# Kernel tuning notes

Hardware: AMD Instinct MI355X
Metric: run time of the kernel (lower is better)

Reference implementation:

```python
import jax, jax.numpy as jnp
import numpy as np

N = 100000      # nodes
E = 1600000     # edges (avg degree 16)
IN = 128        # in_channels
H = 4           # heads
C = 32          # out_channels per head
NEG_SLOPE = 0.2 # PyG GATConv default


def setup_inputs() -> dict:
    key = jax.random.key(0)
    k = jax.random.split(key, 6)
    x = jax.random.normal(k[0], (N, IN), jnp.float32)
    edge_index = jax.random.randint(k[1], (2, E), 0, N, jnp.int32)
    # Learned params of GATConv: linear weight, per-head attention vectors, bias
    W = jax.random.normal(k[2], (IN, H * C), jnp.float32) / np.sqrt(IN)
    a_src = jax.random.normal(k[3], (H, C), jnp.float32) * 0.1
    a_dst = jax.random.normal(k[4], (H, C), jnp.float32) * 0.1
    bias = jnp.zeros((H * C,), jnp.float32)
    return {"x": x, "edge_index": edge_index, "W": W,
            "a_src": a_src, "a_dst": a_dst, "bias": bias}


def reference(x, edge_index, W, a_src, a_dst, bias):
    n = x.shape[0]
    # Linear transform, per-head view: [N, H, C]
    h = (x @ W).reshape(n, H, C)
    # Node-level attention halves: alpha_i = <h_i, a>  -> [N, H]
    alpha_src = jnp.einsum('nhc,hc->nh', h, a_src)
    alpha_dst = jnp.einsum('nhc,hc->nh', h, a_dst)
    # add_self_loops=True (PyG default)
    loops = jnp.arange(n, dtype=edge_index.dtype)
    src = jnp.concatenate([edge_index[0], loops])  # [E+N]
    dst = jnp.concatenate([edge_index[1], loops])
    # Edge attention logits with LeakyReLU: [E+N, H]
    e = jax.nn.leaky_relu(alpha_src[src] + alpha_dst[dst], NEG_SLOPE)
    # Numerically stable softmax over incoming edges of each destination node
    m = jax.ops.segment_max(e, dst, num_segments=n)          # [N, H]
    e = jnp.exp(e - m[dst])
    denom = jax.ops.segment_sum(e, dst, num_segments=n)      # [N, H]
    att = e / denom[dst]                                     # [E+N, H]
    # Weighted scatter-aggregate of source features: [N, H, C]
    out = jax.ops.segment_sum(att[:, :, None] * h[src], dst, num_segments=n)
    # concat=True: flatten heads, add bias
    return out.reshape(n, H * C) + bias
```

## Files before the change

kernel.cpp:

```cpp
#include <hip/hip_runtime.h>
#include <stdint.h>


#define NBLK 512
#define BKT 64
#define CAP 1792

typedef __bf16 bf16x8 __attribute__((ext_vector_type(8)));
typedef float f32x4 __attribute__((ext_vector_type(4)));

__device__ __forceinline__ float lrelu(float x) { return x >= 0.f ? x : 0.2f * x; }
__device__ __forceinline__ float blo(unsigned u) { return __uint_as_float(u << 16); }
__device__ __forceinline__ float bhi(unsigned u) { return __uint_as_float(u & 0xffff0000u); }
__device__ __forceinline__ unsigned pk2(float a, float b) {
  unsigned short ua = __builtin_bit_cast(unsigned short, (__bf16)a);
  unsigned short ub = __builtin_bit_cast(unsigned short, (__bf16)b);
  return ((unsigned)ub << 16) | ua;
}

__global__ __launch_bounds__(256) void k_wprep(const float* __restrict__ W, __bf16* __restrict__ Wt) {
  int idx = blockIdx.x * 256 + threadIdx.x;
  int nn = idx & 127, k = idx >> 7;
  Wt[nn * 128 + k] = (__bf16)W[k * 128 + nn];
}

__global__ __launch_bounds__(256) void k_gemm(const float* __restrict__ x, const __bf16* __restrict__ Wt,
                                              const float* __restrict__ a_src, const float* __restrict__ a_dst,
                                              __bf16* __restrict__ h, float* __restrict__ asrc,
                                              float* __restrict__ adst, int n) {
  __shared__ __align__(16) char Wl[32768];
  __shared__ __align__(16) __bf16 hbuf[4][16 * 128];
  int t = threadIdx.x;
  {
    const float4* s4 = (const float4*)Wt;
    for (int i = t; i < 2048; i += 256) {
      int f = i << 4;
      int nr = f >> 8, c = f & 255;
      *(float4*)(Wl + ((nr << 8) | (c ^ ((nr & 7) << 4)))) = s4[i];
    }
  }
  __syncthreads();
  int wv = t >> 6, lane = t & 63;
  int arow = lane & 15, ag = lane >> 4, c15 = lane & 15;
  float as_t[8], ad_t[8];
#pragma unroll
  for (int tile = 0; tile < 8; ++tile) {
    as_t[tile] = a_src[tile * 16 + c15];
    ad_t[tile] = a_dst[tile * 16 + c15];
  }
  int strip = blockIdx.x * 64 + wv * 16;
  int row = strip + arow;
  float4 fa[8];
  if (row < n) {
    const float4* xr = (const float4*)(x + (size_t)row * 128);
#pragma unroll
    for (int q = 0; q < 4; ++q) {
      fa[2 * q]     = xr[q * 8 + ag * 2];
      fa[2 * q + 1] = xr[q * 8 + ag * 2 + 1];
    }
  } else {
#pragma unroll
    for (int q = 0; q < 8; ++q) fa[q] = make_float4(0.f, 0.f, 0.f, 0.f);
  }
  bf16x8 af[4];
#pragma unroll
  for (int q = 0; q < 4; ++q) {
    af[q][0] = (__bf16)fa[2 * q].x;     af[q][1] = (__bf16)fa[2 * q].y;
    af[q][2] = (__bf16)fa[2 * q].z;     af[q][3] = (__bf16)fa[2 * q].w;
    af[q][4] = (__bf16)fa[2 * q + 1].x; af[q][5] = (__bf16)fa[2 * q + 1].y;
    af[q][6] = (__bf16)fa[2 * q + 1].z; af[q][7] = (__bf16)fa[2 * q + 1].w;
  }
  f32x4 acc[8];
#pragma unroll
  for (int tile = 0; tile < 8; ++tile) acc[tile] = (f32x4){0.f, 0.f, 0.f, 0.f};
#pragma unroll
  for (int q = 0; q < 4; ++q) {
    int gb = (q * 64) + (ag << 4);
#pragma unroll
    for (int tile = 0; tile < 8; ++tile) {
      int nn = tile * 16 + c15;
      bf16x8 bf = *(const bf16x8*)(Wl + ((nn << 8) | (gb ^ ((nn & 7) << 4))));
      acc[tile] = __builtin_amdgcn_mfma_f32_16x16x32_bf16(af[q], bf, acc[tile], 0, 0, 0);
    }
  }
#pragma unroll
  for (int hh = 0; hh < 4; ++hh) {
#pragma unroll
    for (int r = 0; r < 4; ++r) {
      float vps = acc[2 * hh][r] * as_t[2 * hh] + acc[2 * hh + 1][r] * as_t[2 * hh + 1];
      float vpd = acc[2 * hh][r] * ad_t[2 * hh] + acc[2 * hh + 1][r] * ad_t[2 * hh + 1];
#pragma unroll
      for (int m = 1; m < 16; m <<= 1) {
        vps += __shfl_xor(vps, m, 64);
        vpd += __shfl_xor(vpd, m, 64);
      }
      if (c15 == 0) {
        int ro = strip + ag * 4 + r;
        if (ro < n) { asrc[ro * 4 + hh] = vps; adst[ro * 4 + hh] = vpd; }
      }
    }
  }
#pragma unroll
  for (int tile = 0; tile < 8; ++tile) {
#pragma unroll
    for (int r = 0; r < 4; ++r)
      hbuf[wv][(ag * 4 + r) * 128 + tile * 16 + c15] = (__bf16)acc[tile][r];
  }
  int rr = lane >> 2, qq = lane & 3;
  int ro = strip + rr;
  if (ro < n) {
    const float4* src = (const float4*)&hbuf[wv][rr * 128 + qq * 32];
    float4* dst = (float4*)(h + (size_t)ro * 128 + qq * 32);
    dst[0] = src[0];
    dst[1] = src[1];
    dst[2] = src[2];
    dst[3] = src[3];
  }
}


__global__ __launch_bounds__(256) void k_hist(const int* __restrict__ ei, int* __restrict__ cnt2,
                                              int e, int NB, int CE) {
  __shared__ int hist[2048];
  int t = threadIdx.x, blk = blockIdx.x;
  for (int j = t; j < NB; j += 256) hist[j] = 0;
  __syncthreads();
  int i0 = blk * CE, i1 = min(e, i0 + CE);
  for (int i = i0 + t; i < i1; i += 256) atomicAdd(&hist[ei[e + i] >> 6], 1);
  __syncthreads();
  for (int j = t; j < NB; j += 256) cnt2[j * NBLK + blk] = hist[j];
}

__global__ __launch_bounds__(256) void k_scanA(int* __restrict__ cnt2, int* __restrict__ bsums, int m) {
  __shared__ int wsum[4];
  int t = threadIdx.x, i = blockIdx.x * 256 + t;
  int wv = t >> 6, lane = t & 63;
  int v = (i < m) ? cnt2[i] : 0;
  int sc = v;
#pragma unroll
  for (int ofs = 1; ofs < 64; ofs <<= 1) {
    int u = __shfl_up(sc, ofs, 64);
    if (lane >= ofs) sc += u;
  }
  if (lane == 63) wsum[wv] = sc;
  __syncthreads();
  int base = 0;
  for (int w = 0; w < wv; ++w) base += wsum[w];
  if (i < m) cnt2[i] = base + sc - v;
  if (t == 255) bsums[blockIdx.x] = base + sc;
}

__global__ __launch_bounds__(256) void k_scanB(int* __restrict__ bsums, int nbs) {
  __shared__ int wsum[4];
  int t = threadIdx.x, wv = t >> 6, lane = t & 63;
  int carry = 0;
  for (int c = 0; c < nbs; c += 256) {
    int i = c + t;
    int v = (i < nbs) ? bsums[i] : 0;
    int sc = v;
#pragma unroll
    for (int ofs = 1; ofs < 64; ofs <<= 1) {
      int u = __shfl_up(sc, ofs, 64);
      if (lane >= ofs) sc += u;
    }
    if (lane == 63) wsum[wv] = sc;
    __syncthreads();
    int base = carry;
    for (int w = 0; w < wv; ++w) base += wsum[w];
    if (i < nbs) bsums[i] = base + sc - v;
    carry += wsum[0] + wsum[1] + wsum[2] + wsum[3];
    __syncthreads();
  }
}

__global__ __launch_bounds__(256) void k_scanC(int* __restrict__ cnt2, const int* __restrict__ bsums,
                                               int* __restrict__ boffbg, int m, int NB, int e) {
  int i = blockIdx.x * 256 + threadIdx.x;
  if (i < m) {
    int v = cnt2[i] + bsums[i >> 8];
    cnt2[i] = v;
    if ((i & (NBLK - 1)) == 0) boffbg[i / NBLK] = v;
  }
  if (i == 0) boffbg[NB] = e;
}

__global__ __launch_bounds__(256) void k_fill2(const int* __restrict__ ei, const int* __restrict__ cnt2,
                                               unsigned* __restrict__ ebuf, int e, int NB, int CE) {
  __shared__ int cur[2048];
  int t = threadIdx.x, blk = blockIdx.x;
  for (int j = t; j < NB; j += 256) cur[j] = cnt2[j * NBLK + blk];
  __syncthreads();
  int i0 = blk * CE, i1 = min(e, i0 + CE);
  for (int i = i0 + t; i < i1; i += 256) {
    int s = ei[i], d = ei[e + i];
    int pos = atomicAdd(&cur[d >> 6], 1);
    ebuf[pos] = ((unsigned)(d & 63) << 26) | (unsigned)s;
  }
}

__global__ __launch_bounds__(256) void k_agg(const unsigned* __restrict__ ebuf, const int* __restrict__ boffbg,
                                             const float* __restrict__ asrc, const float* __restrict__ adst,
                                             const unsigned* __restrict__ h32, const float* __restrict__ bias,
                                             float* __restrict__ out, int n) {
  __shared__ int sew[CAP];
  __shared__ __align__(8) uint2 psw[CAP];
  __shared__ __align__(16) float adstl[BKT * 4];
  __shared__ int lcnt[BKT], loff[BKT + 1], lcur[BKT];
  int b = blockIdx.x, t = threadIdx.x;
  int wv = t >> 6, lane = t & 63;
  int s0 = boffbg[b], s1 = boffbg[b + 1];
  int cnt = s1 - s0;
  int d0 = b * BKT;
  bool sorted = (cnt <= CAP);
  if (t < BKT) {
    lcnt[t] = 0;
    if (d0 + t < n) ((float4*)adstl)[t] = ((const float4*)adst)[d0 + t];
    else ((float4*)adstl)[t] = make_float4(0.f, 0.f, 0.f, 0.f);
  }
  __syncthreads();
  if (sorted) {
    for (int j = t; j < cnt; j += 256) atomicAdd(&lcnt[ebuf[s0 + j] >> 26], 1);
    __syncthreads();
    if (wv == 0) {
      int v = lcnt[lane];
      int sc = v;
#pragma unroll
      for (int o = 1; o < 64; o <<= 1) {
        int u = __shfl_up(sc, o, 64);
        if (lane >= o) sc += u;
      }
      loff[lane + 1] = sc;
      if (lane == 0) loff[0] = 0;
      lcur[lane] = sc - v;
    }
    __syncthreads();
    for (int j = t; j < cnt; j += 256) {
      unsigned u = ebuf[s0 + j];
      int dl = u >> 26;
      int s = (int)(u & 0x03FFFFFFu);
      float4 as = ((const float4*)asrc)[s];
      float p0 = __expf(lrelu(as.x + adstl[dl * 4 + 0]));
      float p1 = __expf(lrelu(as.y + adstl[dl * 4 + 1]));
      float p2 = __expf(lrelu(as.z + adstl[dl * 4 + 2]));
      float p3 = __expf(lrelu(as.w + adstl[dl * 4 + 3]));
      int pos = atomicAdd(&lcur[dl], 1);
      sew[pos] = s;
      psw[pos] = make_uint2(pk2(p0, p1), pk2(p2, p3));
    }
    __syncthreads();
  }
  int head = lane >> 4;
  bool hodd = (head & 1), hhi = (head & 2);
  float2 bb = ((const float2*)bias)[lane];
  for (int nd = wv; nd < BKT; nd += 4) {
    int d = d0 + nd;
    if (d >= n) break;
    float adh = adstl[nd * 4 + head];
    float pself = __expf(lrelu(asrc[d * 4 + head] + adh));
    unsigned su = h32[((unsigned)d << 6) + lane];
    float acc0 = pself * blo(su), acc1 = pself * bhi(su), dtot = pself;
    if (sorted) {
      int j = loff[nd], j1 = loff[nd + 1];
      for (; j + 4 <= j1; j += 4) {
        int sA = sew[j], sB = sew[j + 1], sC = sew[j + 2], sD = sew[j + 3];
        uint2 wA = psw[j], wB = psw[j + 1], wC = psw[j + 2], wD = psw[j + 3];
        unsigned uA = h32[((unsigned)sA << 6) + lane];
        unsigned uB = h32[((unsigned)sB << 6) + lane];
        unsigned uC = h32[((unsigned)sC << 6) + lane];
        unsigned uD = h32[((unsigned)sD << 6) + lane];
        unsigned vA = hhi ? wA.y : wA.x, vB = hhi ? wB.y : wB.x;
        unsigned vC = hhi ? wC.y : wC.x, vD = hhi ? wD.y : wD.x;
        float pA = hodd ? bhi(vA) : blo(vA);
        float pB = hodd ? bhi(vB) : blo(vB);
        float pC = hodd ? bhi(vC) : blo(vC);
        float pD = hodd ? bhi(vD) : blo(vD);
        dtot += (pA + pB) + (pC + pD);
        acc0 += pA * blo(uA) + pB * blo(uB) + pC * blo(uC) + pD * blo(uD);
        acc1 += pA * bhi(uA) + pB * bhi(uB) + pC * bhi(uC) + pD * bhi(uD);
      }
      for (; j < j1; ++j) {
        int s = sew[j];
        uint2 w = psw[j];
        unsigned u = h32[((unsigned)s << 6) + lane];
        unsigned v = hhi ? w.y : w.x;
        float p = hodd ? bhi(v) : blo(v);
        dtot += p;
        acc0 += p * blo(u);
        acc1 += p * bhi(u);
      }
    } else {
      for (int j = s0; j < s1; ++j) {
        unsigned u = ebuf[j];
        if ((int)(u >> 26) != nd) continue;
        int s = (int)(u & 0x03FFFFFFu);
        unsigned hu = h32[((unsigned)s << 6) + lane];
        float p = __expf(lrelu(asrc[s * 4 + head] + adh));
        dtot += p;
        acc0 += p * blo(hu);
        acc1 += p * bhi(hu);
      }
    }
    float inv = 1.f / dtot;
    ((float2*)(out + (size_t)d * 128))[lane] = make_float2(acc0 * inv + bb.x, acc1 * inv + bb.y);
  }
}

extern "C" void kernel_launch(void* const* d_in, const int* in_sizes, int n_in,
                              void* d_out, int out_size, void* d_ws, size_t ws_size,
                              hipStream_t stream) {
  const float* x     = (const float*)d_in[0];
  const int*   ei    = (const int*)d_in[1];
  const float* W     = (const float*)d_in[2];
  const float* a_src = (const float*)d_in[3];
  const float* a_dst = (const float*)d_in[4];
  const float* bias  = (const float*)d_in[5];
  float* out = (float*)d_out;

  int n = in_sizes[0] / 128;
  int e = in_sizes[1] / 2;
  int NB = (n + BKT - 1) / BKT;
  int m = NB * NBLK;
  int gridA = (m + 255) / 256;
  int CE = (e + NBLK - 1) / NBLK;

  char* ws = (char*)d_ws;
  size_t ofs = 0;
  auto alloc = [&](size_t bytes) { void* p = ws + ofs; ofs = (ofs + bytes + 15) & ~(size_t)15; return p; };
  __bf16* h      = (__bf16*)alloc((size_t)n * 128 * sizeof(__bf16));
  unsigned* h32  = (unsigned*)h;
  float* asrc    = (float*)alloc((size_t)n * 4 * sizeof(float));
  float* adst    = (float*)alloc((size_t)n * 4 * sizeof(float));
  int* cnt2      = (int*)alloc((size_t)m * sizeof(int));
  int* bsums     = (int*)alloc((size_t)gridA * sizeof(int));
  int* boffbg    = (int*)alloc((size_t)(NB + 1) * sizeof(int));
  unsigned* ebuf = (unsigned*)alloc((size_t)e * sizeof(unsigned));
  __bf16* Wt     = (__bf16*)alloc((size_t)128 * 128 * sizeof(__bf16));

  hipLaunchKernelGGL(k_wprep, dim3(64), dim3(256), 0, stream, W, Wt);
  hipLaunchKernelGGL(k_gemm, dim3((n + 63) / 64), dim3(256), 0, stream,
                     x, Wt, a_src, a_dst, h, asrc, adst, n);
  hipLaunchKernelGGL(k_hist, dim3(NBLK), dim3(256), 0, stream, ei, cnt2, e, NB, CE);
  hipLaunchKernelGGL(k_scanA, dim3(gridA), dim3(256), 0, stream, cnt2, bsums, m);
  hipLaunchKernelGGL(k_scanB, dim3(1), dim3(256), 0, stream, bsums, gridA);
  hipLaunchKernelGGL(k_scanC, dim3(gridA), dim3(256), 0, stream, cnt2, bsums, boffbg, m, NB, e);
  hipLaunchKernelGGL(k_fill2, dim3(NBLK), dim3(256), 0, stream, ei, cnt2, ebuf, e, NB, CE);
  hipLaunchKernelGGL(k_agg, dim3(NB), dim3(256), 0, stream,
                     ebuf, boffbg, asrc, adst, h32, bias, out, n);
}
```

Baseline: 199.5 us.

## Split aggregation into CSR-build/softmax kernel and one-wave-per-node gather kernel

The fused per-bucket aggregation kernel is split into two kernels. The first builds a global CSR layout (offsets, adjacency, packed bf16 exp weights) and computes per-node softmax denominators with shared-memory float atomics. The second assigns one wavefront per destination node with an 8-way unrolled feature gather. This removes the LDS capacity limit, the slow unsorted fallback path, and the coarse per-bucket load imbalance. The cost is an extra launch and extra global traffic to write and re-read adjacency and weights (about 12 bytes per edge), plus a float-atomic denominator whose summation order is nondeterministic.

```diff
diff --git a/kernel.cpp b/kernel.cpp
--- a/kernel.cpp
+++ b/kernel.cpp
@@ -4,7 +4,6 @@
 
 #define NBLK 512
 #define BKT 64
-#define CAP 1792
 
 typedef __bf16 bf16x8 __attribute__((ext_vector_type(8)));
 typedef float f32x4 __attribute__((ext_vector_type(4)));
@@ -174,14 +173,15 @@
 }
 
 __global__ __launch_bounds__(256) void k_scanC(int* __restrict__ cnt2, const int* __restrict__ bsums,
-                                               int* __restrict__ boffbg, int m, int NB, int e) {
+                                               int* __restrict__ boffbg, int* __restrict__ off,
+                                               int m, int NB, int n, int e) {
   int i = blockIdx.x * 256 + threadIdx.x;
   if (i < m) {
     int v = cnt2[i] + bsums[i >> 8];
     cnt2[i] = v;
     if ((i & (NBLK - 1)) == 0) boffbg[i / NBLK] = v;
   }
-  if (i == 0) boffbg[NB] = e;
+  if (i == 0) { boffbg[NB] = e; off[n] = e; }
 }
 
 __global__ __launch_bounds__(256) void k_fill2(const int* __restrict__ ei, const int* __restrict__ cnt2,
@@ -198,111 +198,130 @@
   }
 }
 
-__global__ __launch_bounds__(256) void k_agg(const unsigned* __restrict__ ebuf, const int* __restrict__ boffbg,
-                                             const float* __restrict__ asrc, const float* __restrict__ adst,
-                                             const unsigned* __restrict__ h32, const float* __restrict__ bias,
-                                             float* __restrict__ out, int n) {
-  __shared__ int sew[CAP];
-  __shared__ __align__(8) uint2 psw[CAP];
+__global__ __launch_bounds__(256) void k_csr2(const unsigned* __restrict__ ebuf, const int* __restrict__ boffbg,
+                                              const float* __restrict__ asrc, const float* __restrict__ adst,
+                                              int* __restrict__ off, int* __restrict__ adj,
+                                              uint2* __restrict__ pswg, float* __restrict__ inv4,
+                                              float* __restrict__ pself4, int n) {
   __shared__ __align__(16) float adstl[BKT * 4];
-  __shared__ int lcnt[BKT], loff[BKT + 1], lcur[BKT];
+  __shared__ float ldenom[BKT * 4];
+  __shared__ int lcnt[BKT], lcur[BKT];
   int b = blockIdx.x, t = threadIdx.x;
   int wv = t >> 6, lane = t & 63;
   int s0 = boffbg[b], s1 = boffbg[b + 1];
   int cnt = s1 - s0;
   int d0 = b * BKT;
-  bool sorted = (cnt <= CAP);
   if (t < BKT) {
     lcnt[t] = 0;
-    if (d0 + t < n) ((float4*)adstl)[t] = ((const float4*)adst)[d0 + t];
-    else ((float4*)adstl)[t] = make_float4(0.f, 0.f, 0.f, 0.f);
-  }
-  __syncthreads();
-  if (sorted) {
-    for (int j = t; j < cnt; j += 256) atomicAdd(&lcnt[ebuf[s0 + j] >> 26], 1);
-    __syncthreads();
-    if (wv == 0) {
-      int v = lcnt[lane];
-      int sc = v;
-#pragma unroll
-      for (int o = 1; o < 64; o <<= 1) {
-        int u = __shfl_up(sc, o, 64);
-        if (lane >= o) sc += u;
-      }
-      loff[lane + 1] = sc;
-      if (lane == 0) loff[0] = 0;
-      lcur[lane] = sc - v;
-    }
-    __syncthreads();
-    for (int j = t; j < cnt; j += 256) {
-      unsigned u = ebuf[s0 + j];
-      int dl = u >> 26;
-      int s = (int)(u & 0x03FFFFFFu);
-      float4 as = ((const float4*)asrc)[s];
-      float p0 = __expf(lrelu(as.x + adstl[dl * 4 + 0]));
-      float p1 = __expf(lrelu(as.y + adstl[dl * 4 + 1]));
-      float p2 = __expf(lrelu(as.z + adstl[dl * 4 + 2]));
-      float p3 = __expf(lrelu(as.w + adstl[dl * 4 + 3]));
-      int pos = atomicAdd(&lcur[dl], 1);
-      sew[pos] = s;
-      psw[pos] = make_uint2(pk2(p0, p1), pk2(p2, p3));
-    }
-    __syncthreads();
-  }
+    float4 ad = (d0 + t < n) ? ((const float4*)adst)[d0 + t] : make_float4(0.f, 0.f, 0.f, 0.f);
+    ((float4*)adstl)[t] = ad;
+    ldenom[t * 4 + 0] = 0.f; ldenom[t * 4 + 1] = 0.f;
+    ldenom[t * 4 + 2] = 0.f; ldenom[t * 4 + 3] = 0.f;
+  }
+  __syncthreads();
+  for (int j = t; j < cnt; j += 256) atomicAdd(&lcnt[ebuf[s0 + j] >> 26], 1);
+  __syncthreads();
+  if (wv == 0) {
+    int v = lcnt[lane];
+    int sc = v;
+#pragma unroll
+    for (int o = 1; o < 64; o <<= 1) {
+      int u = __shfl_up(sc, o, 64);
+      if (lane >= o) sc += u;
+    }
+    lcur[lane] = sc - v;
+    if (d0 + lane < n) off[d0 + lane] = s0 + sc - v;
+  }
+  __syncthreads();
+  for (int j = t; j < cnt; j += 256) {
+    unsigned u = ebuf[s0 + j];
+    int dl = u >> 26;
+    int s = (int)(u & 0x03FFFFFFu);
+    float4 as = ((const float4*)asrc)[s];
+    float p0 = __expf(lrelu(as.x + adstl[dl * 4 + 0]));
+    float p1 = __expf(lrelu(as.y + adstl[dl * 4 + 1]));
+    float p2 = __expf(lrelu(as.z + adstl[dl * 4 + 2]));
+    float p3 = __expf(lrelu(as.w + adstl[dl * 4 + 3]));
+    int pos = atomicAdd(&lcur[dl], 1);
+    adj[s0 + pos] = s;
+    pswg[s0 + pos] = make_uint2(pk2(p0, p1), pk2(p2, p3));
+    atomicAdd(&ldenom[dl * 4 + 0], p0);
+    atomicAdd(&ldenom[dl * 4 + 1], p1);
+    atomicAdd(&ldenom[dl * 4 + 2], p2);
+    atomicAdd(&ldenom[dl * 4 + 3], p3);
+  }
+  __syncthreads();
+  if (t < BKT && d0 + t < n) {
+    int d = d0 + t;
+    float4 as = ((const float4*)asrc)[d];
+    float4 ps;
+    ps.x = __expf(lrelu(as.x + adstl[t * 4 + 0]));
+    ps.y = __expf(lrelu(as.y + adstl[t * 4 + 1]));
+    ps.z = __expf(lrelu(as.z + adstl[t * 4 + 2]));
+    ps.w = __expf(lrelu(as.w + adstl[t * 4 + 3]));
+    ((float4*)pself4)[d] = ps;
+    float4 iv;
+    iv.x = 1.f / (ldenom[t * 4 + 0] + ps.x);
+    iv.y = 1.f / (ldenom[t * 4 + 1] + ps.y);
+    iv.z = 1.f / (ldenom[t * 4 + 2] + ps.z);
+    iv.w = 1.f / (ldenom[t * 4 + 3] + ps.w);
+    ((float4*)inv4)[d] = iv;
+  }
+}
+
+__global__ __launch_bounds__(256) void k_gather(const int* __restrict__ adj, const int* __restrict__ off,
+                                                const uint2* __restrict__ pswg, const float* __restrict__ inv4,
+                                                const float* __restrict__ pself4, const unsigned* __restrict__ h32,
+                                                const float* __restrict__ bias, float* __restrict__ out, int n) {
+  int gid = blockIdx.x * 256 + threadIdx.x;
+  int node = gid >> 6, lane = gid & 63;
+  if (node >= n) return;
   int head = lane >> 4;
   bool hodd = (head & 1), hhi = (head & 2);
+  int o = off[node], oe = off[node + 1];
+  float inv = inv4[node * 4 + head];
+  float ps = pself4[node * 4 + head];
+  unsigned su = h32[((unsigned)node << 6) + lane];
+  float acc0 = ps * blo(su), acc1 = ps * bhi(su);
+  int j = o;
+  for (; j + 8 <= oe; j += 8) {
+    int sv[8];
+    uint2 wv2[8];
+    unsigned hu[8];
+#pragma unroll
+    for (int k = 0; k < 8; ++k) { sv[k] = adj[j + k]; wv2[k] = pswg[j + k]; }
+#pragma unroll
+    for (int k = 0; k < 8; ++k) hu[k] = h32[((unsigned)sv[k] << 6) + lane];
+#pragma unroll
+    for (int k = 0; k < 8; ++k) {
+      unsigned v = hhi ? wv2[k].y : wv2[k].x;
+      float p = hodd ? bhi(v) : blo(v);
+      acc0 += p * blo(hu[k]);
+      acc1 += p * bhi(hu[k]);
+    }
+  }
+  for (; j + 2 <= oe; j += 2) {
+    int sA = adj[j], sB = adj[j + 1];
+    uint2 wA = pswg[j], wB = pswg[j + 1];
+    unsigned uA = h32[((unsigned)sA << 6) + lane];
+    unsigned uB = h32[((unsigned)sB << 6) + lane];
+    unsigned vA = hhi ? wA.y : wA.x, vB = hhi ? wB.y : wB.x;
+    float pA = hodd ? bhi(vA) : blo(vA);
+    float pB = hodd ? bhi(vB) : blo(vB);
+    acc0 += pA * blo(uA) + pB * blo(uB);
+    acc1 += pA * bhi(uA) + pB * bhi(uB);
+  }
+  if (j < oe) {
+    int s = adj[j];
+    uint2 w = pswg[j];
+    unsigned u = h32[((unsigned)s << 6) + lane];
+    unsigned v = hhi ? w.y : w.x;
+    float p = hodd ? bhi(v) : blo(v);
+    acc0 += p * blo(u);
+    acc1 += p * bhi(u);
+  }
   float2 bb = ((const float2*)bias)[lane];
-  for (int nd = wv; nd < BKT; nd += 4) {
-    int d = d0 + nd;
-    if (d >= n) break;
-    float adh = adstl[nd * 4 + head];
-    float pself = __expf(lrelu(asrc[d * 4 + head] + adh));
-    unsigned su = h32[((unsigned)d << 6) + lane];
-    float acc0 = pself * blo(su), acc1 = pself * bhi(su), dtot = pself;
-    if (sorted) {
-      int j = loff[nd], j1 = loff[nd + 1];
-      for (; j + 4 <= j1; j += 4) {
-        int sA = sew[j], sB = sew[j + 1], sC = sew[j + 2], sD = sew[j + 3];
-        uint2 wA = psw[j], wB = psw[j + 1], wC = psw[j + 2], wD = psw[j + 3];
-        unsigned uA = h32[((unsigned)sA << 6) + lane];
-        unsigned uB = h32[((unsigned)sB << 6) + lane];
-        unsigned uC = h32[((unsigned)sC << 6) + lane];
-        unsigned uD = h32[((unsigned)sD << 6) + lane];
-        unsigned vA = hhi ? wA.y : wA.x, vB = hhi ? wB.y : wB.x;
-        unsigned vC = hhi ? wC.y : wC.x, vD = hhi ? wD.y : wD.x;
-        float pA = hodd ? bhi(vA) : blo(vA);
-        float pB = hodd ? bhi(vB) : blo(vB);
-        float pC = hodd ? bhi(vC) : blo(vC);
-        float pD = hodd ? bhi(vD) : blo(vD);
-        dtot += (pA + pB) + (pC + pD);
-        acc0 += pA * blo(uA) + pB * blo(uB) + pC * blo(uC) + pD * blo(uD);
-        acc1 += pA * bhi(uA) + pB * bhi(uB) + pC * bhi(uC) + pD * bhi(uD);
-      }
-      for (; j < j1; ++j) {
-        int s = sew[j];
-        uint2 w = psw[j];
-        unsigned u = h32[((unsigned)s << 6) + lane];
-        unsigned v = hhi ? w.y : w.x;
-        float p = hodd ? bhi(v) : blo(v);
-        dtot += p;
-        acc0 += p * blo(u);
-        acc1 += p * bhi(u);
-      }
-    } else {
-      for (int j = s0; j < s1; ++j) {
-        unsigned u = ebuf[j];
-        if ((int)(u >> 26) != nd) continue;
-        int s = (int)(u & 0x03FFFFFFu);
-        unsigned hu = h32[((unsigned)s << 6) + lane];
-        float p = __expf(lrelu(asrc[s * 4 + head] + adh));
-        dtot += p;
-        acc0 += p * blo(hu);
-        acc1 += p * bhi(hu);
-      }
-    }
-    float inv = 1.f / dtot;
-    ((float2*)(out + (size_t)d * 128))[lane] = make_float2(acc0 * inv + bb.x, acc1 * inv + bb.y);
-  }
+  ((float2*)(out + (size_t)node * 128))[lane] = make_float2(acc0 * inv + bb.x, acc1 * inv + bb.y);
 }
 
 extern "C" void kernel_launch(void* const* d_in, const int* in_sizes, int n_in,
@@ -330,10 +349,15 @@
   unsigned* h32  = (unsigned*)h;
   float* asrc    = (float*)alloc((size_t)n * 4 * sizeof(float));
   float* adst    = (float*)alloc((size_t)n * 4 * sizeof(float));
+  float* inv4    = (float*)alloc((size_t)n * 4 * sizeof(float));
+  float* pself4  = (float*)alloc((size_t)n * 4 * sizeof(float));
+  int* off       = (int*)alloc((size_t)(n + 1) * sizeof(int));
   int* cnt2      = (int*)alloc((size_t)m * sizeof(int));
   int* bsums     = (int*)alloc((size_t)gridA * sizeof(int));
   int* boffbg    = (int*)alloc((size_t)(NB + 1) * sizeof(int));
   unsigned* ebuf = (unsigned*)alloc((size_t)e * sizeof(unsigned));
+  int* adj       = (int*)alloc((size_t)e * sizeof(int));
+  uint2* pswg    = (uint2*)alloc((size_t)e * sizeof(uint2));
   __bf16* Wt     = (__bf16*)alloc((size_t)128 * 128 * sizeof(__bf16));
 
   hipLaunchKernelGGL(k_wprep, dim3(64), dim3(256), 0, stream, W, Wt);
@@ -342,8 +366,10 @@
   hipLaunchKernelGGL(k_hist, dim3(NBLK), dim3(256), 0, stream, ei, cnt2, e, NB, CE);
   hipLaunchKernelGGL(k_scanA, dim3(gridA), dim3(256), 0, stream, cnt2, bsums, m);
   hipLaunchKernelGGL(k_scanB, dim3(1), dim3(256), 0, stream, bsums, gridA);
-  hipLaunchKernelGGL(k_scanC, dim3(gridA), dim3(256), 0, stream, cnt2, bsums, boffbg, m, NB, e);
+  hipLaunchKernelGGL(k_scanC, dim3(gridA), dim3(256), 0, stream, cnt2, bsums, boffbg, off, m, NB, n, e);
   hipLaunchKernelGGL(k_fill2, dim3(NBLK), dim3(256), 0, stream, ei, cnt2, ebuf, e, NB, CE);
-  hipLaunchKernelGGL(k_agg, dim3(NB), dim3(256), 0, stream,
-                     ebuf, boffbg, asrc, adst, h32, bias, out, n);
-}
+  hipLaunchKernelGGL(k_csr2, dim3(NB), dim3(256), 0, stream, ebuf, boffbg, asrc, adst,
+                     off, adj, pswg, inv4, pself4, n);
+  hipLaunchKernelGGL(k_gather, dim3((n * 64 + 255) / 256), dim3(256), 0, stream,
+                     adj, off, pswg, inv4, pself4, h32, bias, out, n);
+}
```

New measurement: 210.7 us. 1.06x slower.
